# Optimization experiments

Hardware: AMD Instinct MI355X
Metric: run time of the kernel (lower is better)

## Reference

```python
import jax, jax.numpy as jnp
import numpy as np

D_MODEL = 1024
N_HEADS = 16
D_HEAD = D_MODEL // N_HEADS
WIN = 256
NEG_INF = -1e30


def setup_inputs() -> dict:
    key = jax.random.key(0)
    k1, k2, k3 = jax.random.split(key, 3)
    B, L = 4, 4096
    x = jax.random.normal(k1, (B, L, D_MODEL), dtype=jnp.float32)
    w_qkv = jax.random.normal(k2, (D_MODEL, 3 * D_MODEL), dtype=jnp.float32) * (1.0 / np.sqrt(D_MODEL))
    w_out = jax.random.normal(k3, (D_MODEL, D_MODEL), dtype=jnp.float32) * (1.0 / np.sqrt(D_MODEL))
    return {"x": x, "w_qkv": w_qkv, "w_out": w_out}


def _band_mask(nb: int):
    ti = jnp.arange(WIN)[:, None]
    tj = jnp.arange(2 * WIN)[None, :]
    base = (tj >= ti + 1) & (tj <= ti + WIN)
    first = base & (tj >= WIN)                         # block 0 has zero-padded (invalid) prev block
    rest = jnp.broadcast_to(base, (nb - 1, WIN, 2 * WIN))
    return jnp.concatenate([first[None], rest], axis=0)


def reference(x, w_qkv, w_out):
    B, L, D = x.shape
    nb = L // WIN
    qkv = (x @ w_qkv).reshape(B, L, 3, N_HEADS, D_HEAD)
    q, k, v = qkv[:, :, 0], qkv[:, :, 1], qkv[:, :, 2]          # [B, L, H, dh]
    def to_blocks(t):
        return t.transpose(0, 2, 1, 3).reshape(B, N_HEADS, nb, WIN, D_HEAD)
    qb, kb, vb = to_blocks(q), to_blocks(k), to_blocks(v)
    zero_blk = jnp.zeros_like(kb[:, :, :1])
    k_kv = jnp.concatenate([jnp.concatenate([zero_blk, kb[:, :, :-1]], axis=2), kb], axis=3)  # [B,H,nb,2W,dh]
    v_kv = jnp.concatenate([jnp.concatenate([zero_blk, vb[:, :, :-1]], axis=2), vb], axis=3)
    scale = 1.0 / np.sqrt(D_HEAD)
    scores = jnp.einsum('bhnqd,bhnkd->bhnqk', qb, k_kv) * scale
    scores = jnp.where(_band_mask(nb), scores, NEG_INF)
    attn = jax.nn.softmax(scores, axis=-1)
    ob = jnp.einsum('bhnqk,bhnkd->bhnqd', attn, v_kv)
    out = ob.reshape(B, N_HEADS, L, D_HEAD).transpose(0, 2, 1, 3).reshape(B, L, D)
    return out @ w_out
```

## Files before the change

### kernel.cpp

```cpp
#include <hip/hip_runtime.h>

typedef __bf16 bf16_t;
typedef __bf16 bf16x8 __attribute__((ext_vector_type(8)));
typedef float f32x4 __attribute__((ext_vector_type(4)));
typedef unsigned short ushort_t;

#define MFMA_16x16x32(a, b, c) __builtin_amdgcn_mfma_f32_16x16x32_bf16((a), (b), (c), 0, 0, 0)

__device__ __forceinline__ void async_ld16(const void* gptr, void* lptr) {
  typedef __attribute__((address_space(1))) const unsigned int as1_t;
  typedef __attribute__((address_space(3))) unsigned int as3_t;
  __builtin_amdgcn_global_load_lds((as1_t*)(unsigned long long)gptr,
                                   (as3_t*)(unsigned int)(unsigned long long)lptr,
                                   16, 0, 0);
}

__global__ void detect_dtype(const ushort_t* __restrict__ x, int* __restrict__ flag) {
  __shared__ int cnt[256];
  int c = 0;
#pragma unroll
  for (int i = 0; i < 16; ++i) {
    const ushort_t u = x[threadIdx.x * 16 + i];
    const int e = (u >> 7) & 0xFF;
    if ((u & 0x7FFF) != 0 && (e < 0x3A || e > 0xC0)) ++c;
  }
  cnt[threadIdx.x] = c;
  __syncthreads();
  if (threadIdx.x == 0) {
    int t = 0;
    for (int i = 0; i < 256; ++i) t += cnt[i];
    *flag = (t > 512) ? 1 : 0;
  }
}

__global__ __launch_bounds__(256) void convert_to_bf16(const void* __restrict__ src,
                                                       bf16_t* __restrict__ dst, int n8,
                                                       const int* __restrict__ flag) {
  const int isF32 = *flag;
  int i = blockIdx.x * 256 + threadIdx.x;
  const int stride = gridDim.x * 256;
  if (isF32) {
    const float4* s = (const float4*)src;
    for (; i < n8; i += stride) {
      const float4 a = s[(size_t)i * 2];
      const float4 b = s[(size_t)i * 2 + 1];
      bf16x8 o;
      o[0] = (bf16_t)a.x; o[1] = (bf16_t)a.y; o[2] = (bf16_t)a.z; o[3] = (bf16_t)a.w;
      o[4] = (bf16_t)b.x; o[5] = (bf16_t)b.y; o[6] = (bf16_t)b.z; o[7] = (bf16_t)b.w;
      *(bf16x8*)(dst + (size_t)i * 8) = o;
    }
  } else {
    const uint4* s = (const uint4*)src;
    for (; i < n8; i += stride) ((uint4*)dst)[i] = s[i];
  }
}

__global__ __launch_bounds__(256) void transpose_b16(const ushort_t* __restrict__ in,
                                                     ushort_t* __restrict__ out,
                                                     int R, int C) {
  __shared__ alignas(16) ushort_t t[64 * 72];
  const int tid = threadIdx.x;
  const int c0 = blockIdx.x * 64;
  const int r0 = blockIdx.y * 64;
#pragma unroll
  for (int it = 0; it < 2; ++it) {
    int cid = tid + it * 256;
    int row = cid >> 3, co = (cid & 7) * 8;
    *(uint4*)(t + row * 72 + co) = *(const uint4*)(in + (size_t)(r0 + row) * C + c0 + co);
  }
  __syncthreads();
#pragma unroll
  for (int it = 0; it < 2; ++it) {
    int cid = tid + it * 256;
    int orow = cid >> 3, ko = (cid & 7) * 8;
    uint4 u;
    ushort_t* tp = (ushort_t*)&u;
#pragma unroll
    for (int j = 0; j < 8; ++j) tp[j] = t[(ko + j) * 72 + orow];
    *(uint4*)(out + (size_t)(c0 + orow) * R + r0 + ko) = u;
  }
}

__global__ __launch_bounds__(256) void transpose_v(const ushort_t* __restrict__ qkv,
                                                   ushort_t* __restrict__ vT) {
  __shared__ alignas(16) ushort_t t[64 * 72];
  const int tid = threadIdx.x;
  const int l0 = blockIdx.x * 64;
  const int bh = blockIdx.y;
  const int b = bh >> 4, h = bh & 15;
  const ushort_t* src = qkv + ((size_t)(b * 4096 + l0)) * 3072 + 2048 + h * 64;
#pragma unroll
  for (int it = 0; it < 2; ++it) {
    int cid = tid + it * 256;
    int row = cid >> 3, co = (cid & 7) * 8;
    *(uint4*)(t + row * 72 + co) = *(const uint4*)(src + (size_t)row * 3072 + co);
  }
  __syncthreads();
  ushort_t* dst = vT + ((size_t)bh * 64) * 4096 + l0;
#pragma unroll
  for (int it = 0; it < 2; ++it) {
    int cid = tid + it * 256;
    int d = cid >> 3, ko = (cid & 7) * 8;
    uint4 u;
    ushort_t* tp = (ushort_t*)&u;
#pragma unroll
    for (int j = 0; j < 8; ++j) tp[j] = t[(ko + j) * 72 + d];
    *(uint4*)(dst + (size_t)d * 4096 + ko) = u;
  }
}

__global__ __launch_bounds__(512) void gemm_bf16(const bf16_t* __restrict__ A, int lda,
                                                 const bf16_t* __restrict__ Bt,
                                                 void* __restrict__ Cout, int N_out,
                                                 int K, const int* __restrict__ flag) {
  __shared__ alignas(16) bf16_t smem[65536];
  const int tid = threadIdx.x;
  const int wave = tid >> 6;
  const int lane = tid & 63;
  const int l15 = lane & 15;
  const int quad = lane >> 4;
  const int wm = wave >> 2;
  const int wn = wave & 3;

  int lin = blockIdx.y * gridDim.x + blockIdx.x;
  const int nwg = gridDim.x * gridDim.y;
  if ((nwg & 7) == 0) lin = (lin & 7) * (nwg >> 3) + (lin >> 3);
  const int tn = (lin % gridDim.x) * 256;
  const int tm = (lin / gridDim.x) * 256;

  f32x4 acc[8][4];
#pragma unroll
  for (int i = 0; i < 8; ++i)
#pragma unroll
    for (int j = 0; j < 4; ++j) acc[i][j] = (f32x4){0.f, 0.f, 0.f, 0.f};

  const int r_st = tid >> 3;
  const int jg8 = ((tid & 7) ^ (r_st & 7)) * 8;
  const int wofs = wave * 512;

  const int rowA = wm * 16 + l15;
  const int rowB = wn * 16 + l15;
  const int sw = l15 & 7;
  const int c0 = (quad ^ sw) * 8;
  const int c1 = ((quad | 4) ^ sw) * 8;

  const int NT = K >> 6;

#define STAGE_HALF(G, ldg, grow0, kk, ldsbase)                              \
  do {                                                                      \
    const bf16_t* _g = (G) + (size_t)((grow0) + r_st) * (ldg) + (kk) + jg8; \
    async_ld16(_g, &smem[(ldsbase) + wofs]);                                \
    async_ld16(_g + (size_t)64 * (ldg), &smem[(ldsbase) + 4096 + wofs]);    \
  } while (0)

#define READ_A(mh)                                                \
  do {                                                            \
    _Pragma("unroll") for (int q = 0; q < 4; ++q) {               \
      const int off = bufA + (((mh)*128 + q * 32 + rowA) << 6);   \
      a_[q][0] = *(const bf16x8*)&smem[off + c0];                 \
      a_[q][1] = *(const bf16x8*)&smem[off + c1];                 \
    }                                                             \
  } while (0)

#define READ_B(nh)                                                \
  do {                                                            \
    _Pragma("unroll") for (int jn = 0; jn < 2; ++jn) {            \
      const int off = bufB + (((nh)*128 + jn * 64 + rowB) << 6);  \
      b_[jn][0] = *(const bf16x8*)&smem[off + c0];                \
      b_[jn][1] = *(const bf16x8*)&smem[off + c1];                \
    }                                                             \
  } while (0)

#define DO_MFMA(mh, nh)                                                      \
  do {                                                                       \
    _Pragma("unroll") for (int q = 0; q < 4; ++q)                            \
        _Pragma("unroll") for (int jn = 0; jn < 2; ++jn) {                   \
      acc[(mh)*4 + q][(nh)*2 + jn] =                                         \
          MFMA_16x16x32(a_[q][0], b_[jn][0], acc[(mh)*4 + q][(nh)*2 + jn]);  \
      acc[(mh)*4 + q][(nh)*2 + jn] =                                         \
          MFMA_16x16x32(a_[q][1], b_[jn][1], acc[(mh)*4 + q][(nh)*2 + jn]);  \
    }                                                                        \
  } while (0)

#define PHASE_MID(VMC)                                     \
  asm volatile("s_waitcnt vmcnt(" VMC ")" ::: "memory");   \
  __builtin_amdgcn_s_barrier();                            \
  asm volatile("s_waitcnt lgkmcnt(0)" ::: "memory");       \
  __builtin_amdgcn_sched_barrier(0);                       \
  __builtin_amdgcn_s_setprio(1)

#define PHASE_END()               \
  __builtin_amdgcn_s_setprio(0);  \
  __builtin_amdgcn_s_barrier();   \
  __builtin_amdgcn_sched_barrier(0)

  STAGE_HALF(A, lda, tm, 0, 0);
  STAGE_HALF(Bt, K, tn, 0, 16384);
  STAGE_HALF(Bt, K, tn + 128, 0, 16384 + 8192);
  STAGE_HALF(A, lda, tm + 128, 0, 8192);
  asm volatile("s_waitcnt vmcnt(4)" ::: "memory");
  __builtin_amdgcn_s_barrier();

  bf16x8 a_[4][2], b_[2][2];
  int bufA = 0;
  for (int t = 0; t < NT; ++t) {
    const int bufB = bufA + 16384;
    const int sA = bufA ^ 32768;
    const int sB = sA + 16384;
    int kst = (t + 1) << 6;
    if (kst == K) kst = 0;

    READ_A(0);
    READ_B(0);
    STAGE_HALF(A, lda, tm, kst, sA);
    PHASE_MID("4");
    DO_MFMA(0, 0);
    PHASE_END();

    READ_B(1);
    STAGE_HALF(Bt, K, tn, kst, sB);
    PHASE_MID("4");
    DO_MFMA(0, 1);
    PHASE_END();

    READ_A(1);
    STAGE_HALF(Bt, K, tn + 128, kst, sB + 8192);
    PHASE_MID("6");
    DO_MFMA(1, 1);
    PHASE_END();

    READ_B(0);
    STAGE_HALF(A, lda, tm + 128, kst, sA + 8192);
    PHASE_MID("4");
    DO_MFMA(1, 0);
    PHASE_END();

    bufA ^= 32768;
  }

  asm volatile("s_waitcnt vmcnt(0)" ::: "memory");
  __syncthreads();

  const int isF32 = flag ? *flag : 0;
  if (isF32) {
#pragma unroll
    for (int f = 0; f < 8; ++f) {
      const int m0 = tm + (f >> 2) * 128 + (f & 3) * 32 + wm * 16 + quad * 4;
#pragma unroll
      for (int nidx = 0; nidx < 4; ++nidx) {
        const int col = tn + (nidx >> 1) * 128 + (nidx & 1) * 64 + wn * 16 + l15;
        float* cp = (float*)Cout + (size_t)m0 * N_out + col;
#pragma unroll
        for (int r = 0; r < 4; ++r) cp[(size_t)r * N_out] = acc[f][nidx][r];
      }
    }
  } else {
    bf16_t* stg = smem + wave * 1152;
#pragma unroll
    for (int f = 0; f < 8; ++f) {
#pragma unroll
      for (int nidx = 0; nidx < 4; ++nidx)
#pragma unroll
        for (int r = 0; r < 4; ++r)
          stg[(quad * 4 + r) * 72 + nidx * 16 + l15] = (bf16_t)acc[f][nidx][r];
      __asm__ volatile("s_waitcnt lgkmcnt(0)" ::: "memory");
      const int m0 = tm + (f >> 2) * 128 + (f & 3) * 32 + wm * 16;
#pragma unroll
      for (int p = 0; p < 2; ++p) {
        const int idx = lane + p * 64;
        const int row = idx >> 3, c8 = (idx & 7) * 8;
        uint4 u = *(const uint4*)(stg + row * 72 + c8);
        const int col = tn + ((c8 >> 5) << 7) + (((c8 >> 4) & 1) << 6) + wn * 16 + (c8 & 15);
        *(uint4*)((bf16_t*)Cout + (size_t)(m0 + row) * N_out + col) = u;
      }
      __asm__ volatile("s_waitcnt lgkmcnt(0)" ::: "memory");
    }
  }
#undef STAGE_HALF
#undef READ_A
#undef READ_B
#undef DO_MFMA
#undef PHASE_MID
#undef PHASE_END
}

__global__ __launch_bounds__(256) void attn_swa(bf16_t* qkv, const bf16_t* __restrict__ vT) {
  __shared__ alignas(16) bf16_t k_lds[64 * 72];
  __shared__ alignas(16) bf16_t vt_lds[64 * 72];
  __shared__ alignas(16) bf16_t p_lds[4 * 16 * 72];

  const int wg = blockIdx.x;
  const int b = wg >> 10;
  const int h = (wg >> 6) & 15;
  const int qt = wg & 63;
  const int blk = qt >> 2;
  const int wq = qt & 3;
  const int tid = threadIdx.x;
  const int wave = tid >> 6;
  const int lane = tid & 63;
  const int l15 = lane & 15;
  const int quad = lane >> 4;
  const int qw = qt * 64 + wave * 16;

  const size_t qoff = ((size_t)(b * 4096 + qw + l15)) * 3072 + h * 64;
  const bf16x8 qf0 = *(const bf16x8*)(qkv + qoff + quad * 8);
  const bf16x8 qf1 = *(const bf16x8*)(qkv + qoff + 32 + quad * 8);

  f32x4 of[4];
#pragma unroll
  for (int i = 0; i < 4; ++i) of[i] = (f32x4){0.f, 0.f, 0.f, 0.f};
  float m_i[4], l_i[4];
#pragma unroll
  for (int r = 0; r < 4; ++r) {
    m_i[r] = -1e30f;
    l_i[r] = 0.0f;
  }

  const int kb0 = blk * 256 - 256;
  const int kclo = (blk == 0) ? 4 : wq;
  const int kchi = wq + 4;

  for (int kc = kclo; kc <= kchi; ++kc) {
    const int kb = kb0 + kc * 64;
    __syncthreads();
#pragma unroll
    for (int it = 0; it < 2; ++it) {
      int cid = tid + it * 256;
      int row = cid >> 3;
      int co = (cid & 7) * 8;
      *(uint4*)(k_lds + row * 72 + co) =
          *(const uint4*)(qkv + ((size_t)(b * 4096 + kb + row)) * 3072 + 1024 + h * 64 + co);
      *(uint4*)(vt_lds + row * 72 + co) =
          *(const uint4*)(vT + (((size_t)b * 16 + h) * 64 + row) * 4096 + kb + co);
    }
    __syncthreads();

    f32x4 s[4];
#pragma unroll
    for (int nt = 0; nt < 4; ++nt) {
      bf16x8 kf0 = *(const bf16x8*)(k_lds + (nt * 16 + l15) * 72 + quad * 8);
      bf16x8 kf1 = *(const bf16x8*)(k_lds + (nt * 16 + l15) * 72 + 32 + quad * 8);
      f32x4 z = (f32x4){0.f, 0.f, 0.f, 0.f};
      z = MFMA_16x16x32(qf0, kf0, z);
      z = MFMA_16x16x32(qf1, kf1, z);
      s[nt] = z;
    }

    float sv[4][4];
#pragma unroll
    for (int nt = 0; nt < 4; ++nt) {
      const int key = kb + nt * 16 + l15;
#pragma unroll
      for (int r = 0; r < 4; ++r) {
        const int p = qw + quad * 4 + r;
        const bool valid = (key <= p) && (key + 256 > p);
        sv[nt][r] = valid ? s[nt][r] * 0.125f : -1e30f;
      }
    }
    float rm[4];
#pragma unroll
    for (int r = 0; r < 4; ++r)
      rm[r] = fmaxf(fmaxf(sv[0][r], sv[1][r]), fmaxf(sv[2][r], sv[3][r]));
#pragma unroll
    for (int off = 1; off < 16; off <<= 1)
#pragma unroll
      for (int r = 0; r < 4; ++r) rm[r] = fmaxf(rm[r], __shfl_xor(rm[r], off));

    float mn[4], alpha[4];
#pragma unroll
    for (int r = 0; r < 4; ++r) {
      mn[r] = fmaxf(m_i[r], rm[r]);
      alpha[r] = __expf(m_i[r] - mn[r]);
      m_i[r] = mn[r];
    }

    float rs[4] = {0.f, 0.f, 0.f, 0.f};
#pragma unroll
    for (int nt = 0; nt < 4; ++nt)
#pragma unroll
      for (int r = 0; r < 4; ++r) {
        const float pv = (sv[nt][r] > -1e29f) ? __expf(sv[nt][r] - mn[r]) : 0.0f;
        rs[r] += pv;
        p_lds[wave * 1152 + (quad * 4 + r) * 72 + nt * 16 + l15] = (bf16_t)pv;
      }
#pragma unroll
    for (int off = 1; off < 16; off <<= 1)
#pragma unroll
      for (int r = 0; r < 4; ++r) rs[r] += __shfl_xor(rs[r], off);
#pragma unroll
    for (int r = 0; r < 4; ++r) l_i[r] = l_i[r] * alpha[r] + rs[r];
#pragma unroll
    for (int dt = 0; dt < 4; ++dt)
#pragma unroll
      for (int r = 0; r < 4; ++r) of[dt][r] *= alpha[r];

    __syncthreads();

#pragma unroll
    for (int kk = 0; kk < 2; ++kk) {
      bf16x8 pf = *(const bf16x8*)(p_lds + wave * 1152 + l15 * 72 + kk * 32 + quad * 8);
#pragma unroll
      for (int dt = 0; dt < 4; ++dt) {
        bf16x8 vf = *(const bf16x8*)(vt_lds + (dt * 16 + l15) * 72 + kk * 32 + quad * 8);
        of[dt] = MFMA_16x16x32(pf, vf, of[dt]);
      }
    }
  }

  float inv[4];
#pragma unroll
  for (int r = 0; r < 4; ++r) inv[r] = 1.0f / fmaxf(l_i[r], 1e-20f);
  bf16_t* op = qkv + ((size_t)(b * 4096 + qw)) * 3072 + h * 64;
#pragma unroll
  for (int dt = 0; dt < 4; ++dt)
#pragma unroll
    for (int r = 0; r < 4; ++r)
      op[(size_t)(quad * 4 + r) * 3072 + dt * 16 + l15] = (bf16_t)(of[dt][r] * inv[r]);
}

extern "C" void kernel_launch(void* const* d_in, const int* in_sizes, int n_in,
                              void* d_out, int out_size, void* d_ws, size_t ws_size,
                              hipStream_t stream) {
  char* ws = (char*)d_ws;
  bf16_t* wTq = (bf16_t*)(ws);
  bf16_t* wTo = (bf16_t*)(ws + 6291456);
  bf16_t* qkv = (bf16_t*)(ws + 8388608);
  int* flag = (int*)(ws + 109051904);

  bf16_t* xb = (bf16_t*)d_out;
  bf16_t* vTb = (bf16_t*)d_out;
  bf16_t* tmpq = qkv;
  bf16_t* tmpo = qkv + 3145728;

  detect_dtype<<<1, 256, 0, stream>>>((const ushort_t*)d_in[0], flag);
  convert_to_bf16<<<1024, 256, 0, stream>>>(d_in[0], xb, 2097152, flag);
  convert_to_bf16<<<512, 256, 0, stream>>>(d_in[1], tmpq, 393216, flag);
  convert_to_bf16<<<256, 256, 0, stream>>>(d_in[2], tmpo, 131072, flag);
  transpose_b16<<<dim3(48, 16), 256, 0, stream>>>((const ushort_t*)tmpq, (ushort_t*)wTq,
                                                  1024, 3072);
  transpose_b16<<<dim3(16, 16), 256, 0, stream>>>((const ushort_t*)tmpo, (ushort_t*)wTo,
                                                  1024, 1024);
  gemm_bf16<<<dim3(12, 64), 512, 0, stream>>>(xb, 1024, wTq, qkv, 3072, 1024, nullptr);
  transpose_v<<<dim3(64, 64), 256, 0, stream>>>((const ushort_t*)qkv, (ushort_t*)vTb);
  attn_swa<<<dim3(4096), 256, 0, stream>>>(qkv, vTb);
  gemm_bf16<<<dim3(4, 64), 512, 0, stream>>>(qkv, 3072, wTo, d_out, 1024, 1024, flag);
}
```

Before: 380.2 us.

## Prefetch attention KV into registers and keep both GEMM B fragments live

In the GEMM main loop, both B fragment halves are now held in separate registers, so the fourth phase no longer re-reads B from LDS. The useless wrap-around prefetch on the last K iteration is skipped. In the attention kernel, the next K/V chunk is loaded into registers while the current one is processed, and workgroup indices are remapped to interleave batches and heads. The kernel also raises wave priority around the MFMA sections and drops a block-wide barrier before the P·V step, since each wave only reads its own P tile. The cost is extra VGPR pressure in both kernels, which could reduce occupancy.

```diff
diff --git a/kernel.cpp b/kernel.cpp
--- a/kernel.cpp
+++ b/kernel.cpp
@@ -162,23 +162,23 @@
     }                                                             \
   } while (0)
 
-#define READ_B(nh)                                                \
+#define READ_B(nh, dst)                                           \
   do {                                                            \
     _Pragma("unroll") for (int jn = 0; jn < 2; ++jn) {            \
       const int off = bufB + (((nh)*128 + jn * 64 + rowB) << 6);  \
-      b_[jn][0] = *(const bf16x8*)&smem[off + c0];                \
-      b_[jn][1] = *(const bf16x8*)&smem[off + c1];                \
+      dst[jn][0] = *(const bf16x8*)&smem[off + c0];               \
+      dst[jn][1] = *(const bf16x8*)&smem[off + c1];               \
     }                                                             \
   } while (0)
 
-#define DO_MFMA(mh, nh)                                                      \
+#define DO_MFMA(mh, nh, bb)                                                  \
   do {                                                                       \
     _Pragma("unroll") for (int q = 0; q < 4; ++q)                            \
         _Pragma("unroll") for (int jn = 0; jn < 2; ++jn) {                   \
       acc[(mh)*4 + q][(nh)*2 + jn] =                                         \
-          MFMA_16x16x32(a_[q][0], b_[jn][0], acc[(mh)*4 + q][(nh)*2 + jn]);  \
+          MFMA_16x16x32(a_[q][0], bb[jn][0], acc[(mh)*4 + q][(nh)*2 + jn]);  \
       acc[(mh)*4 + q][(nh)*2 + jn] =                                         \
-          MFMA_16x16x32(a_[q][1], b_[jn][1], acc[(mh)*4 + q][(nh)*2 + jn]);  \
+          MFMA_16x16x32(a_[q][1], bb[jn][1], acc[(mh)*4 + q][(nh)*2 + jn]);  \
     }                                                                        \
   } while (0)
 
@@ -189,6 +189,12 @@
   __builtin_amdgcn_sched_barrier(0);                       \
   __builtin_amdgcn_s_setprio(1)
 
+#define PHASE_MID_NV()                                     \
+  __builtin_amdgcn_s_barrier();                            \
+  asm volatile("s_waitcnt lgkmcnt(0)" ::: "memory");       \
+  __builtin_amdgcn_sched_barrier(0);                       \
+  __builtin_amdgcn_s_setprio(1)
+
 #define PHASE_END()               \
   __builtin_amdgcn_s_setprio(0);  \
   __builtin_amdgcn_s_barrier();   \
@@ -201,38 +207,37 @@
   asm volatile("s_waitcnt vmcnt(4)" ::: "memory");
   __builtin_amdgcn_s_barrier();
 
-  bf16x8 a_[4][2], b_[2][2];
+  bf16x8 a_[4][2], b0_[2][2], b1_[2][2];
   int bufA = 0;
   for (int t = 0; t < NT; ++t) {
     const int bufB = bufA + 16384;
     const int sA = bufA ^ 32768;
     const int sB = sA + 16384;
-    int kst = (t + 1) << 6;
-    if (kst == K) kst = 0;
+    const int kst = (t + 1) << 6;
+    const bool pf = (kst < K);
 
     READ_A(0);
-    READ_B(0);
-    STAGE_HALF(A, lda, tm, kst, sA);
+    READ_B(0, b0_);
+    if (pf) STAGE_HALF(A, lda, tm, kst, sA);
     PHASE_MID("4");
-    DO_MFMA(0, 0);
+    DO_MFMA(0, 0, b0_);
     PHASE_END();
 
-    READ_B(1);
-    STAGE_HALF(Bt, K, tn, kst, sB);
+    READ_B(1, b1_);
+    if (pf) STAGE_HALF(Bt, K, tn, kst, sB);
     PHASE_MID("4");
-    DO_MFMA(0, 1);
+    DO_MFMA(0, 1, b1_);
     PHASE_END();
 
     READ_A(1);
-    STAGE_HALF(Bt, K, tn + 128, kst, sB + 8192);
+    if (pf) STAGE_HALF(Bt, K, tn + 128, kst, sB + 8192);
+    PHASE_MID_NV();
+    DO_MFMA(1, 1, b1_);
+    PHASE_END();
+
+    if (pf) STAGE_HALF(A, lda, tm + 128, kst, sA + 8192);
     PHASE_MID("6");
-    DO_MFMA(1, 1);
-    PHASE_END();
-
-    READ_B(0);
-    STAGE_HALF(A, lda, tm + 128, kst, sA + 8192);
-    PHASE_MID("4");
-    DO_MFMA(1, 0);
+    DO_MFMA(1, 0, b0_);
     PHASE_END();
 
     bufA ^= 32768;
@@ -281,6 +286,7 @@
 #undef READ_B
 #undef DO_MFMA
 #undef PHASE_MID
+#undef PHASE_MID_NV
 #undef PHASE_END
 }
 
@@ -289,7 +295,8 @@
   __shared__ alignas(16) bf16_t vt_lds[64 * 72];
   __shared__ alignas(16) bf16_t p_lds[4 * 16 * 72];
 
-  const int wg = blockIdx.x;
+  int wg = blockIdx.x;
+  wg = (wg & 7) * 512 + (wg >> 3);
   const int b = wg >> 10;
   const int h = (wg >> 6) & 15;
   const int qt = wg & 63;
@@ -320,22 +327,34 @@
   const int kclo = (blk == 0) ? 4 : wq;
   const int kchi = wq + 4;
 
+  const int row0 = tid >> 3;
+  const int co8 = (tid & 7) * 8;
+  const bf16_t* kbase = qkv + ((size_t)b * 4096) * 3072 + 1024 + h * 64;
+  const bf16_t* vbase = vT + (((size_t)b * 16 + h) * 64) * 4096;
+  uint4 kr0, kr1, vr0, vr1;
+
+#define ISSUE_KV(KB)                                                           \
+  do {                                                                         \
+    kr0 = *(const uint4*)(kbase + (size_t)((KB) + row0) * 3072 + co8);         \
+    kr1 = *(const uint4*)(kbase + (size_t)((KB) + row0 + 32) * 3072 + co8);    \
+    vr0 = *(const uint4*)(vbase + (size_t)row0 * 4096 + (KB) + co8);           \
+    vr1 = *(const uint4*)(vbase + (size_t)(row0 + 32) * 4096 + (KB) + co8);    \
+  } while (0)
+
+  ISSUE_KV(kb0 + kclo * 64);
+
   for (int kc = kclo; kc <= kchi; ++kc) {
     const int kb = kb0 + kc * 64;
     __syncthreads();
-#pragma unroll
-    for (int it = 0; it < 2; ++it) {
-      int cid = tid + it * 256;
-      int row = cid >> 3;
-      int co = (cid & 7) * 8;
-      *(uint4*)(k_lds + row * 72 + co) =
-          *(const uint4*)(qkv + ((size_t)(b * 4096 + kb + row)) * 3072 + 1024 + h * 64 + co);
-      *(uint4*)(vt_lds + row * 72 + co) =
-          *(const uint4*)(vT + (((size_t)b * 16 + h) * 64 + row) * 4096 + kb + co);
-    }
+    *(uint4*)(k_lds + row0 * 72 + co8) = kr0;
+    *(uint4*)(k_lds + (row0 + 32) * 72 + co8) = kr1;
+    *(uint4*)(vt_lds + row0 * 72 + co8) = vr0;
+    *(uint4*)(vt_lds + (row0 + 32) * 72 + co8) = vr1;
+    if (kc < kchi) ISSUE_KV(kb + 64);
     __syncthreads();
 
     f32x4 s[4];
+    __builtin_amdgcn_s_setprio(1);
 #pragma unroll
     for (int nt = 0; nt < 4; ++nt) {
       bf16x8 kf0 = *(const bf16x8*)(k_lds + (nt * 16 + l15) * 72 + quad * 8);
@@ -345,6 +364,7 @@
       z = MFMA_16x16x32(qf1, kf1, z);
       s[nt] = z;
     }
+    __builtin_amdgcn_s_setprio(0);
 
     float sv[4][4];
 #pragma unroll
@@ -394,8 +414,7 @@
 #pragma unroll
       for (int r = 0; r < 4; ++r) of[dt][r] *= alpha[r];
 
-    __syncthreads();
-
+    __builtin_amdgcn_s_setprio(1);
 #pragma unroll
     for (int kk = 0; kk < 2; ++kk) {
       bf16x8 pf = *(const bf16x8*)(p_lds + wave * 1152 + l15 * 72 + kk * 32 + quad * 8);
@@ -405,7 +424,9 @@
         of[dt] = MFMA_16x16x32(pf, vf, of[dt]);
       }
     }
-  }
+    __builtin_amdgcn_s_setprio(0);
+  }
+#undef ISSUE_KV
 
   float inv[4];
 #pragma unroll
```

Result: faster. 365.1 us (-4.0%).
